# Performance work log

Hardware: AMD Instinct MI355X
Metric: run time of the kernel (lower is better)

The kernel has to match this reference:

```python
import jax, jax.numpy as jnp
import numpy as np

D_MODEL = 1024
NUM_HEADS = 16
D_K = D_MODEL // NUM_HEADS


def setup_inputs() -> dict:
    key = jax.random.key(0)
    ks = jax.random.split(key, 11)
    B, S = 4, 2048
    s = 1.0 / np.sqrt(D_MODEL)
    inp = {
        'q': jax.random.normal(ks[0], (B, S, D_MODEL), dtype=jnp.float32),
        'k': jax.random.normal(ks[1], (B, S, D_MODEL), dtype=jnp.float32),
        'v': jax.random.normal(ks[2], (B, S, D_MODEL), dtype=jnp.float32),
        'Wq': jax.random.normal(ks[3], (D_MODEL, D_MODEL), dtype=jnp.float32) * s,
        'bq': jnp.zeros((D_MODEL,), dtype=jnp.float32),
        'Wk': jax.random.normal(ks[4], (D_MODEL, D_MODEL), dtype=jnp.float32) * s,
        'bk': jnp.zeros((D_MODEL,), dtype=jnp.float32),
        'Wv': jax.random.normal(ks[5], (D_MODEL, D_MODEL), dtype=jnp.float32) * s,
        'bv': jnp.zeros((D_MODEL,), dtype=jnp.float32),
        'Wo': jax.random.normal(ks[6], (D_MODEL, D_MODEL), dtype=jnp.float32) * s,
        'bo': jnp.zeros((D_MODEL,), dtype=jnp.float32),
    }
    return inp


def _split_heads(x):
    B, S, _ = x.shape
    return x.reshape(B, S, NUM_HEADS, D_K).transpose(0, 2, 1, 3)  # [B,H,S,d_k]


def reference(q, k, v, Wq, bq, Wk, bk, Wv, bv, Wo, bo):
    B, S, _ = q.shape
    qh = _split_heads(q @ Wq.T + bq)
    kh = _split_heads(k @ Wk.T + bk)
    vh = _split_heads(v @ Wv.T + bv)
    scale = 1.0 / jnp.sqrt(jnp.asarray(D_K, dtype=qh.dtype))
    scores = jnp.einsum('bhqd,bhkd->bhqk', qh, kh) * scale  # [B,H,S,S]
    attn = jax.nn.softmax(scores, axis=-1)
    out = jnp.einsum('bhqk,bhkd->bhqd', attn, vh)  # [B,H,S,d_k]
    out = out.transpose(0, 2, 1, 3).reshape(B, S, D_MODEL)
    return out @ Wo.T + bo
```

## Files before the change

### kernel.cpp

```cpp
#include <hip/hip_runtime.h>


typedef __bf16 bf16_t;
typedef bf16_t bf16x8 __attribute__((ext_vector_type(8)));
typedef bf16_t bf16x4 __attribute__((ext_vector_type(4)));
typedef float  f32x4  __attribute__((ext_vector_type(4)));
typedef short  s16x4  __attribute__((ext_vector_type(4)));

#define MFMA16(A, B, C) __builtin_amdgcn_mfma_f32_16x16x32_bf16(A, B, C, 0, 0, 0)

static __device__ __forceinline__ f32x4 mfma16k16(bf16x4 a, bf16x4 b, f32x4 c) {
  return __builtin_amdgcn_mfma_f32_16x16x16bf16_1k(
      __builtin_bit_cast(s16x4, a), __builtin_bit_cast(s16x4, b), c, 0, 0, 0);
}

#define NB   4
#define SEQ  2048
#define DM   1024
#define NH   16
#define DK   64
#define MTOT (NB * SEQ)
#define QSCALE 0.18033688011112042f

__device__ __forceinline__ void async_copy16(bf16_t* lds, const bf16_t* gsrc) {
  __builtin_amdgcn_global_load_lds(
      (const __attribute__((address_space(1))) unsigned int*)gsrc,
      (__attribute__((address_space(3))) unsigned int*)lds, 16, 0, 0);
}

__device__ __forceinline__ float fast_exp2(float x) {
#if __has_builtin(__builtin_amdgcn_exp2f)
  return __builtin_amdgcn_exp2f(x);
#else
  return exp2f(x);
#endif
}

__global__ __launch_bounds__(256) void cvt3(const float* __restrict__ a,
                                            const float* __restrict__ b,
                                            const float* __restrict__ c,
                                            bf16_t* __restrict__ oa,
                                            bf16_t* __restrict__ ob,
                                            bf16_t* __restrict__ oc, int n4) {
  const int z = blockIdx.y;
  const float* s = (z == 0) ? a : (z == 1) ? b : c;
  bf16_t* d = (z == 0) ? oa : (z == 1) ? ob : oc;
  int i = blockIdx.x * 256 + threadIdx.x;
  if (i < n4) {
    f32x4 v = ((const f32x4*)s)[i];
    ((bf16x4*)d)[i] = __builtin_convertvector(v, bf16x4);
  }
}

__global__ __launch_bounds__(256) void cvt4(const float* __restrict__ a,
                                            const float* __restrict__ b,
                                            const float* __restrict__ c,
                                            const float* __restrict__ dd,
                                            bf16_t* __restrict__ oa,
                                            bf16_t* __restrict__ ob,
                                            bf16_t* __restrict__ oc,
                                            bf16_t* __restrict__ od, int n4) {
  const int z = blockIdx.y;
  const float* s = (z == 0) ? a : (z == 1) ? b : (z == 2) ? c : dd;
  bf16_t* d = (z == 0) ? oa : (z == 1) ? ob : (z == 2) ? oc : od;
  int i = blockIdx.x * 256 + threadIdx.x;
  if (i < n4) {
    f32x4 v = ((const f32x4*)s)[i];
    ((bf16x4*)d)[i] = __builtin_convertvector(v, bf16x4);
  }
}

__device__ __forceinline__ void gemm_core_1024(const bf16_t* __restrict__ A,
                                               const bf16_t* __restrict__ W,
                                               bf16_t* sA, bf16_t* sB,
                                               f32x4 (&acc)[4][4], int m0, int n0) {
  const int tid = threadIdx.x;
  const int lane = tid & 63, r = lane & 15, qd = lane >> 4;
  const int wave = tid >> 6;
  const int wm = (wave & 1) * 64, wn = (wave >> 1) * 64;
  const int arow = tid >> 2, achk = (tid & 3) * 8;
  const bf16_t* gA = A + (size_t)(m0 + arow) * DM + achk;
  const bf16_t* gB = W + (size_t)(n0 + arow) * DM + achk;
  bf16_t* lA = sA + arow * 32 + achk;
  bf16_t* lB = sB + arow * 32 + achk;

#define GSTAGE(buf, k0)                                                       \
  do {                                                                        \
    async_copy16(lA + (buf) * 4096,           gA + (k0));                     \
    async_copy16(lA + (buf) * 4096 + 64 * 32, gA + (k0) + (size_t)64 * DM);   \
    async_copy16(lB + (buf) * 4096,           gB + (k0));                     \
    async_copy16(lB + (buf) * 4096 + 64 * 32, gB + (k0) + (size_t)64 * DM);   \
  } while (0)

  GSTAGE(0, 0);
#pragma unroll 2
  for (int k0 = 0; k0 < DM; k0 += 32) {
    const int buf = (k0 >> 5) & 1;
    __syncthreads();
    if (k0 + 32 < DM) GSTAGE(buf ^ 1, k0 + 32);

    const bf16_t* cA = sA + buf * 4096;
    const bf16_t* cB = sB + buf * 4096;
    bf16x8 af[4], bw[4];
#pragma unroll
    for (int i = 0; i < 4; i++)
      af[i] = *(const bf16x8*)(cA + (wm + i * 16 + r) * 32 + qd * 8);
#pragma unroll
    for (int j = 0; j < 4; j++)
      bw[j] = *(const bf16x8*)(cB + (wn + j * 16 + r) * 32 + qd * 8);
#pragma unroll
    for (int i = 0; i < 4; i++)
#pragma unroll
      for (int j = 0; j < 4; j++)
        acc[i][j] = MFMA16(af[i], bw[j], acc[i][j]);
  }
#undef GSTAGE
}

__global__ __launch_bounds__(256)
void gemm_qkv(const bf16_t* __restrict__ qb, const bf16_t* __restrict__ kb,
              const bf16_t* __restrict__ vb, const bf16_t* __restrict__ wq,
              const bf16_t* __restrict__ wk, const bf16_t* __restrict__ wv,
              const float* __restrict__ bq, const float* __restrict__ bk,
              const float* __restrict__ bv, bf16_t* __restrict__ Qh,
              bf16_t* __restrict__ Kh, bf16_t* __restrict__ Vt) {
  __shared__ __align__(16) bf16_t sA[2 * 128 * 32];
  __shared__ __align__(16) bf16_t sB[2 * 128 * 32];
  const int z = blockIdx.z;
  const bf16_t* A = (z == 0) ? qb : (z == 1) ? kb : vb;
  const bf16_t* W = (z == 0) ? wq : (z == 1) ? wk : wv;
  const float* bias = (z == 0) ? bq : (z == 1) ? bk : bv;
  const int m0 = blockIdx.x * 128, n0 = blockIdx.y * 128;

  f32x4 acc[4][4] = {};
  gemm_core_1024(A, W, sA, sB, acc, m0, n0);

  const int tid = threadIdx.x, lane = tid & 63, r = lane & 15, qd = lane >> 4;
  const int wave = tid >> 6, wm = (wave & 1) * 64, wn = (wave >> 1) * 64;
#pragma unroll
  for (int j = 0; j < 4; j++) {
    const int n = n0 + wn + j * 16 + r;
    const float bs = bias[n];
    const int h = n >> 6, d = n & 63;
#pragma unroll
    for (int i = 0; i < 4; i++) {
#pragma unroll
      for (int rr = 0; rr < 4; rr++) {
        const int m = m0 + wm + i * 16 + qd * 4 + rr;
        const int b_ = m >> 11, s_ = m & 2047;
        float v = acc[i][j][rr] + bs;
        if (z == 0) {
          v *= QSCALE;
          Qh[(((size_t)b_ * NH + h) * SEQ + s_) * DK + d] = (bf16_t)v;
        } else if (z == 1) {
          Kh[(((size_t)b_ * NH + h) * SEQ + s_) * DK + d] = (bf16_t)v;
        } else {
          Vt[(((size_t)b_ * NH + h) * DK + d) * SEQ + (s_ ^ ((d & 1) * 4))] =
              (bf16_t)v;
        }
      }
    }
  }
}

__global__ __launch_bounds__(256)
void gemm_out(const bf16_t* __restrict__ A, const bf16_t* __restrict__ W,
              const float* __restrict__ bias, float* __restrict__ C) {
  __shared__ __align__(16) bf16_t sA[2 * 128 * 32];
  __shared__ __align__(16) bf16_t sB[2 * 128 * 32];
  const int m0 = blockIdx.x * 128, n0 = blockIdx.y * 128;
  f32x4 acc[4][4] = {};
  gemm_core_1024(A, W, sA, sB, acc, m0, n0);

  const int tid = threadIdx.x, lane = tid & 63, r = lane & 15, qd = lane >> 4;
  const int wave = tid >> 6, wm = (wave & 1) * 64, wn = (wave >> 1) * 64;
#pragma unroll
  for (int j = 0; j < 4; j++) {
    const int n = n0 + wn + j * 16 + r;
    const float bs = bias[n];
#pragma unroll
    for (int i = 0; i < 4; i++) {
#pragma unroll
      for (int rr = 0; rr < 4; rr++) {
        const int m = m0 + wm + i * 16 + qd * 4 + rr;
        C[(size_t)m * DM + n] = acc[i][j][rr] + bs;
      }
    }
  }
}

__global__ __launch_bounds__(256)
void attn(const bf16_t* __restrict__ Qh, const bf16_t* __restrict__ Kh,
          const bf16_t* __restrict__ Vt, bf16_t* __restrict__ Ah) {
  __shared__ __align__(16) bf16_t sK[2][128 * 64];
  __shared__ __align__(16) bf16_t sV[2][64 * 128];

  const int tid = threadIdx.x, wave = tid >> 6, lane = tid & 63;
  const int r = lane & 15, qd = lane >> 4;
  const int id = blockIdx.x;
  const int xcd = id & 7, sub = id >> 3;
  const int bh = xcd * 8 + (sub >> 4);
  const int q0 = (sub & 15) * 128 + wave * 32;
  const size_t bK = (size_t)bh * SEQ * DK;
  const size_t bV = (size_t)bh * DK * SEQ;

  bf16x8 aq[2][2];
#pragma unroll
  for (int qt = 0; qt < 2; qt++)
#pragma unroll
    for (int hf = 0; hf < 2; hf++)
      aq[qt][hf] = *(const bf16x8*)(Qh + bK + (size_t)(q0 + qt * 16 + r) * DK +
                                    hf * 32 + qd * 8);

  f32x4 o[4][2] = {};
  f32x4 lacc[2] = {};
  bf16x4 vone;
#pragma unroll
  for (int i = 0; i < 4; i++) vone[i] = (bf16_t)1.0f;

  const int krow = tid >> 3, kc = tid & 7;
  const int vrow = tid >> 4, vc = tid & 15;

  const bf16_t* gK = Kh + bK + (size_t)krow * DK + ((kc ^ (krow & 7)) * 8);
  const bf16_t* gV = Vt + bV + (size_t)vrow * SEQ + ((vc ^ ((vrow >> 1) & 7)) * 8);

#define STAGE(buf, kv0)                                                        \
  do {                                                                         \
    _Pragma("unroll") for (int it_ = 0; it_ < 4; it_++)                        \
        async_copy16(&sK[buf][0] + it_ * 2048 + tid * 8,                       \
                     gK + (size_t)(kv0 + it_ * 32) * DK);                      \
    _Pragma("unroll") for (int it_ = 0; it_ < 4; it_++)                        \
        async_copy16(&sV[buf][0] + it_ * 2048 + tid * 8,                       \
                     gV + (size_t)it_ * 16 * SEQ + (kv0));                     \
  } while (0)

  STAGE(0, 0);

  for (int it = 0; it < 16; it++) {
    const int buf = it & 1;
    __syncthreads();
    if (it < 15) STAGE(buf ^ 1, (it + 1) * 128);

    const bf16_t* K0 = &sK[buf][0];
    const bf16_t* V0 = &sV[buf][0];

    f32x4 s[2][8];
#pragma unroll
    for (int mt = 0; mt < 8; mt++) {
      const int row = mt * 16 + r;
      bf16x8 ka0 = *(const bf16x8*)(K0 + row * 64 + ((qd ^ (r & 7)) * 8));
      bf16x8 ka1 = *(const bf16x8*)(K0 + row * 64 + (((4 + qd) ^ (r & 7)) * 8));
#pragma unroll
      for (int qt = 0; qt < 2; qt++) {
        f32x4 t = {0.f, 0.f, 0.f, 0.f};
        t = MFMA16(ka0, aq[qt][0], t);
        t = MFMA16(ka1, aq[qt][1], t);
        s[qt][mt] = t;
      }
    }

    bf16x4 p[2][8];
#pragma unroll
    for (int qt = 0; qt < 2; qt++) {
#pragma unroll
      for (int mt = 0; mt < 8; mt++) {
        f32x4 e;
#pragma unroll
        for (int rr = 0; rr < 4; rr++) e[rr] = fast_exp2(s[qt][mt][rr]);
        p[qt][mt] = __builtin_convertvector(e, bf16x4);
        lacc[qt] = mfma16k16(vone, p[qt][mt], lacc[qt]);
      }
    }

#pragma unroll
    for (int dt = 0; dt < 4; dt++) {
      const int d = dt * 16 + r;
#pragma unroll
      for (int mt = 0; mt < 8; mt++) {
        bf16x4 va = *(const bf16x4*)(V0 + d * 128 + (((mt * 4 + qd) ^ r) * 4));
#pragma unroll
        for (int qt = 0; qt < 2; qt++)
          o[dt][qt] = mfma16k16(va, p[qt][mt], o[dt][qt]);
      }
    }
  }

  const float linv0 = 1.0f / lacc[0][0];
  const float linv1 = 1.0f / lacc[1][0];
  const int b_ = bh >> 4, h_ = bh & 15;
#pragma unroll
  for (int qt = 0; qt < 2; qt++) {
    const float linv = qt ? linv1 : linv0;
    const size_t rowbase = ((size_t)b_ * SEQ + q0 + qt * 16 + r) * DM + h_ * DK;
#pragma unroll
    for (int dt = 0; dt < 4; dt++) {
      f32x4 w = o[dt][qt] * linv;
      *(bf16x4*)(Ah + rowbase + dt * 16 + qd * 4) =
          __builtin_convertvector(w, bf16x4);
    }
  }
}

extern "C" void kernel_launch(void* const* d_in, const int* in_sizes, int n_in,
                              void* d_out, int out_size, void* d_ws,
                              size_t ws_size, hipStream_t stream) {
  const float* q  = (const float*)d_in[0];
  const float* k  = (const float*)d_in[1];
  const float* v  = (const float*)d_in[2];
  const float* Wq = (const float*)d_in[3];
  const float* bq = (const float*)d_in[4];
  const float* Wk = (const float*)d_in[5];
  const float* bk = (const float*)d_in[6];
  const float* Wv = (const float*)d_in[7];
  const float* bv = (const float*)d_in[8];
  const float* Wo = (const float*)d_in[9];
  const float* bo = (const float*)d_in[10];

  char* ws = (char*)d_ws;
  const size_t SZ_QKV = (size_t)MTOT * DM * 2;
  const size_t SZ_W   = (size_t)DM * DM * 2;
  bf16_t* qb  = (bf16_t*)(ws);
  bf16_t* kb_ = (bf16_t*)(ws + SZ_QKV);
  bf16_t* vb  = (bf16_t*)(ws + 2 * SZ_QKV);
  bf16_t* Wqb = (bf16_t*)(ws + 3 * SZ_QKV);
  bf16_t* Wkb = (bf16_t*)(ws + 3 * SZ_QKV + SZ_W);
  bf16_t* Wvb = (bf16_t*)(ws + 3 * SZ_QKV + 2 * SZ_W);
  bf16_t* Wob = (bf16_t*)(ws + 3 * SZ_QKV + 3 * SZ_W);
  bf16_t* Qh  = (bf16_t*)(ws + 3 * SZ_QKV + 4 * SZ_W);
  bf16_t* Kh  = (bf16_t*)(ws + 4 * SZ_QKV + 4 * SZ_W);
  bf16_t* Vt  = (bf16_t*)(ws + 5 * SZ_QKV + 4 * SZ_W);
  bf16_t* Ah  = (bf16_t*)(ws + 6 * SZ_QKV + 4 * SZ_W);

  const int n4_qkv = MTOT * DM / 4;
  const int n4_w   = DM * DM / 4;
  cvt3<<<dim3(n4_qkv / 256, 3), 256, 0, stream>>>(q, k, v, qb, kb_, vb, n4_qkv);
  cvt4<<<dim3(n4_w / 256, 4), 256, 0, stream>>>(Wq, Wk, Wv, Wo, Wqb, Wkb, Wvb,
                                                Wob, n4_w);

  gemm_qkv<<<dim3(64, 8, 3), 256, 0, stream>>>(qb, kb_, vb, Wqb, Wkb, Wvb, bq,
                                               bk, bv, Qh, Kh, Vt);

  attn<<<dim3(1024), 256, 0, stream>>>(Qh, Kh, Vt, Ah);

  gemm_out<<<dim3(64, 8), 256, 0, stream>>>(Ah, Wob, bo, (float*)d_out);
}
```

Before: 378.4 us.

## Enlarge GEMM tiles to 256x128 and read V directly from global in attention

The projection GEMMs now use 256x128 block tiles, with each wave computing 128x64 and a larger A staging buffer, and occupancy is hinted with launch_bounds(256,2). The goal is more reuse per loaded tile and half as many blocks. In attention, V is no longer staged through LDS: each lane loads its V fragments straight from global memory (unswizzled Vt layout), which drops LDS traffic and copies but leans on cache and uncoalesced 8-byte loads. The larger accumulator raises register pressure, and the output GEMM grid shrinks to 256 blocks, which may underfill the GPU.

```diff
diff --git a/kernel.cpp b/kernel.cpp
--- a/kernel.cpp
+++ b/kernel.cpp
@@ -73,23 +73,25 @@
 __device__ __forceinline__ void gemm_core_1024(const bf16_t* __restrict__ A,
                                                const bf16_t* __restrict__ W,
                                                bf16_t* sA, bf16_t* sB,
-                                               f32x4 (&acc)[4][4], int m0, int n0) {
+                                               f32x4 (&acc)[8][4], int m0, int n0) {
   const int tid = threadIdx.x;
   const int lane = tid & 63, r = lane & 15, qd = lane >> 4;
   const int wave = tid >> 6;
-  const int wm = (wave & 1) * 64, wn = (wave >> 1) * 64;
+  const int wm = (wave & 1) * 128, wn = (wave >> 1) * 64;
   const int arow = tid >> 2, achk = (tid & 3) * 8;
   const bf16_t* gA = A + (size_t)(m0 + arow) * DM + achk;
   const bf16_t* gB = W + (size_t)(n0 + arow) * DM + achk;
   bf16_t* lA = sA + arow * 32 + achk;
   bf16_t* lB = sB + arow * 32 + achk;
 
-#define GSTAGE(buf, k0)                                                       \
-  do {                                                                        \
-    async_copy16(lA + (buf) * 4096,           gA + (k0));                     \
-    async_copy16(lA + (buf) * 4096 + 64 * 32, gA + (k0) + (size_t)64 * DM);   \
-    async_copy16(lB + (buf) * 4096,           gB + (k0));                     \
-    async_copy16(lB + (buf) * 4096 + 64 * 32, gB + (k0) + (size_t)64 * DM);   \
+#define GSTAGE(buf, k0)                                                        \
+  do {                                                                         \
+    _Pragma("unroll") for (int t_ = 0; t_ < 4; t_++)                           \
+        async_copy16(lA + (buf) * 8192 + t_ * 2048,                            \
+                     gA + (k0) + (size_t)(t_ * 64) * DM);                      \
+    _Pragma("unroll") for (int t_ = 0; t_ < 2; t_++)                           \
+        async_copy16(lB + (buf) * 4096 + t_ * 2048,                            \
+                     gB + (k0) + (size_t)(t_ * 64) * DM);                      \
   } while (0)
 
   GSTAGE(0, 0);
@@ -99,17 +101,17 @@
     __syncthreads();
     if (k0 + 32 < DM) GSTAGE(buf ^ 1, k0 + 32);
 
-    const bf16_t* cA = sA + buf * 4096;
+    const bf16_t* cA = sA + buf * 8192;
     const bf16_t* cB = sB + buf * 4096;
-    bf16x8 af[4], bw[4];
-#pragma unroll
-    for (int i = 0; i < 4; i++)
+    bf16x8 af[8], bw[4];
+#pragma unroll
+    for (int i = 0; i < 8; i++)
       af[i] = *(const bf16x8*)(cA + (wm + i * 16 + r) * 32 + qd * 8);
 #pragma unroll
     for (int j = 0; j < 4; j++)
       bw[j] = *(const bf16x8*)(cB + (wn + j * 16 + r) * 32 + qd * 8);
 #pragma unroll
-    for (int i = 0; i < 4; i++)
+    for (int i = 0; i < 8; i++)
 #pragma unroll
       for (int j = 0; j < 4; j++)
         acc[i][j] = MFMA16(af[i], bw[j], acc[i][j]);
@@ -117,33 +119,33 @@
 #undef GSTAGE
 }
 
-__global__ __launch_bounds__(256)
+__global__ __launch_bounds__(256, 2)
 void gemm_qkv(const bf16_t* __restrict__ qb, const bf16_t* __restrict__ kb,
               const bf16_t* __restrict__ vb, const bf16_t* __restrict__ wq,
               const bf16_t* __restrict__ wk, const bf16_t* __restrict__ wv,
               const float* __restrict__ bq, const float* __restrict__ bk,
               const float* __restrict__ bv, bf16_t* __restrict__ Qh,
               bf16_t* __restrict__ Kh, bf16_t* __restrict__ Vt) {
-  __shared__ __align__(16) bf16_t sA[2 * 128 * 32];
+  __shared__ __align__(16) bf16_t sA[2 * 256 * 32];
   __shared__ __align__(16) bf16_t sB[2 * 128 * 32];
   const int z = blockIdx.z;
   const bf16_t* A = (z == 0) ? qb : (z == 1) ? kb : vb;
   const bf16_t* W = (z == 0) ? wq : (z == 1) ? wk : wv;
   const float* bias = (z == 0) ? bq : (z == 1) ? bk : bv;
-  const int m0 = blockIdx.x * 128, n0 = blockIdx.y * 128;
-
-  f32x4 acc[4][4] = {};
+  const int m0 = blockIdx.x * 256, n0 = blockIdx.y * 128;
+
+  f32x4 acc[8][4] = {};
   gemm_core_1024(A, W, sA, sB, acc, m0, n0);
 
   const int tid = threadIdx.x, lane = tid & 63, r = lane & 15, qd = lane >> 4;
-  const int wave = tid >> 6, wm = (wave & 1) * 64, wn = (wave >> 1) * 64;
+  const int wave = tid >> 6, wm = (wave & 1) * 128, wn = (wave >> 1) * 64;
 #pragma unroll
   for (int j = 0; j < 4; j++) {
     const int n = n0 + wn + j * 16 + r;
     const float bs = bias[n];
     const int h = n >> 6, d = n & 63;
 #pragma unroll
-    for (int i = 0; i < 4; i++) {
+    for (int i = 0; i < 8; i++) {
 #pragma unroll
       for (int rr = 0; rr < 4; rr++) {
         const int m = m0 + wm + i * 16 + qd * 4 + rr;
@@ -155,31 +157,30 @@
         } else if (z == 1) {
           Kh[(((size_t)b_ * NH + h) * SEQ + s_) * DK + d] = (bf16_t)v;
         } else {
-          Vt[(((size_t)b_ * NH + h) * DK + d) * SEQ + (s_ ^ ((d & 1) * 4))] =
-              (bf16_t)v;
+          Vt[(((size_t)b_ * NH + h) * DK + d) * SEQ + s_] = (bf16_t)v;
         }
       }
     }
   }
 }
 
-__global__ __launch_bounds__(256)
+__global__ __launch_bounds__(256, 2)
 void gemm_out(const bf16_t* __restrict__ A, const bf16_t* __restrict__ W,
               const float* __restrict__ bias, float* __restrict__ C) {
-  __shared__ __align__(16) bf16_t sA[2 * 128 * 32];
+  __shared__ __align__(16) bf16_t sA[2 * 256 * 32];
   __shared__ __align__(16) bf16_t sB[2 * 128 * 32];
-  const int m0 = blockIdx.x * 128, n0 = blockIdx.y * 128;
-  f32x4 acc[4][4] = {};
+  const int m0 = blockIdx.x * 256, n0 = blockIdx.y * 128;
+  f32x4 acc[8][4] = {};
   gemm_core_1024(A, W, sA, sB, acc, m0, n0);
 
   const int tid = threadIdx.x, lane = tid & 63, r = lane & 15, qd = lane >> 4;
-  const int wave = tid >> 6, wm = (wave & 1) * 64, wn = (wave >> 1) * 64;
+  const int wave = tid >> 6, wm = (wave & 1) * 128, wn = (wave >> 1) * 64;
 #pragma unroll
   for (int j = 0; j < 4; j++) {
     const int n = n0 + wn + j * 16 + r;
     const float bs = bias[n];
 #pragma unroll
-    for (int i = 0; i < 4; i++) {
+    for (int i = 0; i < 8; i++) {
 #pragma unroll
       for (int rr = 0; rr < 4; rr++) {
         const int m = m0 + wm + i * 16 + qd * 4 + rr;
@@ -193,7 +194,6 @@
 void attn(const bf16_t* __restrict__ Qh, const bf16_t* __restrict__ Kh,
           const bf16_t* __restrict__ Vt, bf16_t* __restrict__ Ah) {
   __shared__ __align__(16) bf16_t sK[2][128 * 64];
-  __shared__ __align__(16) bf16_t sV[2][64 * 128];
 
   const int tid = threadIdx.x, wave = tid >> 6, lane = tid & 63;
   const int r = lane & 15, qd = lane >> 4;
@@ -219,30 +219,24 @@
   for (int i = 0; i < 4; i++) vone[i] = (bf16_t)1.0f;
 
   const int krow = tid >> 3, kc = tid & 7;
-  const int vrow = tid >> 4, vc = tid & 15;
-
   const bf16_t* gK = Kh + bK + (size_t)krow * DK + ((kc ^ (krow & 7)) * 8);
-  const bf16_t* gV = Vt + bV + (size_t)vrow * SEQ + ((vc ^ ((vrow >> 1) & 7)) * 8);
 
 #define STAGE(buf, kv0)                                                        \
   do {                                                                         \
     _Pragma("unroll") for (int it_ = 0; it_ < 4; it_++)                        \
         async_copy16(&sK[buf][0] + it_ * 2048 + tid * 8,                       \
                      gK + (size_t)(kv0 + it_ * 32) * DK);                      \
-    _Pragma("unroll") for (int it_ = 0; it_ < 4; it_++)                        \
-        async_copy16(&sV[buf][0] + it_ * 2048 + tid * 8,                       \
-                     gV + (size_t)it_ * 16 * SEQ + (kv0));                     \
   } while (0)
 
   STAGE(0, 0);
 
   for (int it = 0; it < 16; it++) {
     const int buf = it & 1;
+    const int kv0 = it * 128;
     __syncthreads();
-    if (it < 15) STAGE(buf ^ 1, (it + 1) * 128);
+    if (it < 15) STAGE(buf ^ 1, kv0 + 128);
 
     const bf16_t* K0 = &sK[buf][0];
-    const bf16_t* V0 = &sV[buf][0];
 
     f32x4 s[2][8];
 #pragma unroll
@@ -274,14 +268,17 @@
 
 #pragma unroll
     for (int dt = 0; dt < 4; dt++) {
-      const int d = dt * 16 + r;
-#pragma unroll
-      for (int mt = 0; mt < 8; mt++) {
-        bf16x4 va = *(const bf16x4*)(V0 + d * 128 + (((mt * 4 + qd) ^ r) * 4));
+      const bf16_t* vptr =
+          Vt + bV + (size_t)(dt * 16 + r) * SEQ + kv0 + qd * 4;
+      bf16x4 va[8];
+#pragma unroll
+      for (int mt = 0; mt < 8; mt++)
+        va[mt] = *(const bf16x4*)(vptr + mt * 16);
+#pragma unroll
+      for (int mt = 0; mt < 8; mt++)
 #pragma unroll
         for (int qt = 0; qt < 2; qt++)
-          o[dt][qt] = mfma16k16(va, p[qt][mt], o[dt][qt]);
-      }
+          o[dt][qt] = mfma16k16(va[mt], p[qt][mt], o[dt][qt]);
     }
   }
 
@@ -337,10 +334,10 @@
   cvt4<<<dim3(n4_w / 256, 4), 256, 0, stream>>>(Wq, Wk, Wv, Wo, Wqb, Wkb, Wvb,
                                                 Wob, n4_w);
 
-  gemm_qkv<<<dim3(64, 8, 3), 256, 0, stream>>>(qb, kb_, vb, Wqb, Wkb, Wvb, bq,
+  gemm_qkv<<<dim3(32, 8, 3), 256, 0, stream>>>(qb, kb_, vb, Wqb, Wkb, Wvb, bq,
                                                bk, bv, Qh, Kh, Vt);
 
   attn<<<dim3(1024), 256, 0, stream>>>(Qh, Kh, Vt, Ah);
 
-  gemm_out<<<dim3(64, 8), 256, 0, stream>>>(Ah, Wob, bo, (float*)d_out);
-}
+  gemm_out<<<dim3(32, 8), 256, 0, stream>>>(Ah, Wob, bo, (float*)d_out);
+}
```

Measured after the change: 531.3 us. +40.4%, slower.
